# Performance work log

Measured on AMD Instinct MI355X. Metric: run time of the kernel, lower is better.

The kernel has to match this reference:

```python
import jax, jax.numpy as jnp
from jax import lax
import numpy as np


def _box_sum(x, k):
    # zero-padded sliding-window sum over last two dims of [B, H, W];
    # 'SAME' padding with additive identity 0 exactly matches nn.Unfold's
    # zero padding of k//2 on each side for odd k.
    return lax.reduce_window(x, 0.0, lax.add, (1, k, k), (1, 1, 1), 'SAME')


def _local_std(x, k):
    # torch.std over the k*k patch dim is the unbiased (n-1) sample std;
    # fused one-pass form: var = (sum(x^2) - sum(x)^2/n) / (n-1)
    n = float(k * k)
    s1 = _box_sum(x, k)
    s2 = _box_sum(x * x, k)
    var = (s2 - s1 * s1 / n) / (n - 1.0)
    return jnp.sqrt(jnp.maximum(var, 0.0))


def setup_inputs() -> dict:
    key = jax.random.key(0)
    k1, k2 = jax.random.split(key)
    B, C, H, W = 8, 6, 1024, 1024
    predictions = jax.random.normal(k1, (B, C, H, W), dtype=jnp.float32)
    targets = jax.random.randint(k2, (B, H, W), 0, C, dtype=jnp.int64)
    return {"predictions": predictions, "targets": targets, "kernel_size": 5}


def reference(predictions, targets, kernel_size):
    k = int(kernel_size)
    pred_classes = jnp.argmax(predictions, axis=1).astype(jnp.float32)  # [B,H,W]
    tgt = targets.astype(jnp.float32)                                    # [B,H,W]
    pred_consistency = _local_std(pred_classes, k)
    target_consistency = _local_std(tgt, k)
    return jnp.mean((pred_consistency - target_consistency) ** 2)
```

## Files before the change

### kernel.cpp

```cpp
#include <hip/hip_runtime.h>

#define IMG_H 1024
#define IMG_W 1024
#define HW    (IMG_H * IMG_W)
#define HW4   (HW / 4)
#define NCLS  6
#define NBATCH 8
#define TH 8
#define HR 12
#define CSW 1032

__global__ __launch_bounds__(256, 4) void fused_loss_kernel(
    const float* __restrict__ pred, const int* __restrict__ tgt,
    float* __restrict__ out) {
  __shared__ unsigned int halo32[HR * 256];
  __shared__ unsigned int colsum[4 * CSW];
  __shared__ float wsum[4];

  const int tid = threadIdx.x;
  const int job = (blockIdx.x & 7) * 128 + (blockIdx.x >> 3);
  const int img = job >> 7;
  const int y0  = (job & 127) * TH;
  const float* pimg = pred + (size_t)img * NCLS * HW;
  const int*   timg = tgt  + (size_t)img * HW;

  if (tid < 32) {
    const int r = tid >> 3, j = tid & 7;
    colsum[r * CSW + ((j < 4) ? j : 1024 + j)] = 0u;
  }

  for (int k = 0; k < HR * 256; k += 256) {
    const int id  = k + tid;
    const int row = id >> 8;
    const int g   = id & 255;
    const int gy  = y0 + row - 2;
    unsigned int w = 0u;
    if ((unsigned)gy < IMG_H) {
      const float4* p = (const float4*)(pimg + (size_t)gy * IMG_W) + g;
      float4 best = p[0];
      int cx = 0, cy = 0, cz = 0, cw = 0;
#pragma unroll
      for (int c = 1; c < NCLS; ++c) {
        const float4 v = p[(size_t)c * HW4];
        if (v.x > best.x) { best.x = v.x; cx = c; }
        if (v.y > best.y) { best.y = v.y; cy = c; }
        if (v.z > best.z) { best.z = v.z; cz = c; }
        if (v.w > best.w) { best.w = v.w; cw = c; }
      }
      const int4 t4 = *((const int4*)(timg + (size_t)gy * IMG_W) + g);
      w = (unsigned)(cx | (t4.x << 3))
        | ((unsigned)(cy | (t4.y << 3)) << 8)
        | ((unsigned)(cz | (t4.z << 3)) << 16)
        | ((unsigned)(cw | (t4.w << 3)) << 24);
    }
    halo32[row * 256 + g] = w;
  }
  __syncthreads();

  float acc = 0.f;
#pragma unroll
  for (int bb = 0; bb < 2; ++bb) {
    for (int k = 0; k < 4 * 256; k += 256) {
      const int id = k + tid;
      const int r  = id >> 8;
      const int g  = id & 255;
      const unsigned int* h = &halo32[(bb * 4 + r) * 256 + g];
      unsigned s1p[4] = {0,0,0,0}, s2p[4] = {0,0,0,0};
      unsigned s1t[4] = {0,0,0,0}, s2t[4] = {0,0,0,0};
#pragma unroll
      for (int d = 0; d < 5; ++d) {
        const unsigned wv = h[d * 256];
#pragma unroll
        for (int j = 0; j < 4; ++j) {
          const unsigned pv = (wv >> (8 * j)) & 7u;
          const unsigned tv = (wv >> (8 * j + 3)) & 7u;
          s1p[j] += pv; s2p[j] += pv * pv;
          s1t[j] += tv; s2t[j] += tv * tv;
        }
      }
      uint4 o;
      o.x = s1p[0] | (s2p[0] << 8) | (s1t[0] << 16) | (s2t[0] << 24);
      o.y = s1p[1] | (s2p[1] << 8) | (s1t[1] << 16) | (s2t[1] << 24);
      o.z = s1p[2] | (s2p[2] << 8) | (s1t[2] << 16) | (s2t[2] << 24);
      o.w = s1p[3] | (s2p[3] << 8) | (s1t[3] << 16) | (s2t[3] << 24);
      *(uint4*)&colsum[r * CSW + 4 + 4 * g] = o;
    }
    __syncthreads();

    for (int k = 0; k < 4 * 256; k += 256) {
      const int id = k + tid;
      const int r  = id >> 8;
      const int g  = id & 255;
      const unsigned int* cs = &colsum[r * CSW + 4 * g];
      const uint4 wa = *(const uint4*)(cs);
      const uint4 wb = *(const uint4*)(cs + 4);
      const uint4 wc = *(const uint4*)(cs + 8);
      const unsigned w[12] = {wa.x, wa.y, wa.z, wa.w,
                              wb.x, wb.y, wb.z, wb.w,
                              wc.x, wc.y, wc.z, wc.w};
#pragma unroll
      for (int j = 0; j < 4; ++j) {
        int s1p = 0, s2p = 0, s1t = 0, s2t = 0;
#pragma unroll
        for (int d = 0; d < 5; ++d) {
          const unsigned v = w[j + 2 + d];
          s1p += (int)(v & 0xFFu);
          s2p += (int)((v >> 8) & 0xFFu);
          s1t += (int)((v >> 16) & 0xFFu);
          s2t += (int)(v >> 24);
        }
        const float varp = (float)(25 * s2p - s1p * s1p) * (1.0f / 600.0f);
        const float vart = (float)(25 * s2t - s1t * s1t) * (1.0f / 600.0f);
        const float dd = sqrtf(varp) - sqrtf(vart);
        acc += dd * dd;
      }
    }
    __syncthreads();
  }

#pragma unroll
  for (int off = 32; off > 0; off >>= 1) acc += __shfl_down(acc, off, 64);
  const int lane = tid & 63;
  const int wid  = tid >> 6;
  if (lane == 0) wsum[wid] = acc;
  __syncthreads();
  if (tid == 0) {
    const float t = wsum[0] + wsum[1] + wsum[2] + wsum[3];
    atomicAdd(out, t * (1.0f / 8388608.0f));
  }
}

extern "C" void kernel_launch(void* const* d_in, const int* in_sizes, int n_in,
                              void* d_out, int out_size, void* d_ws, size_t ws_size,
                              hipStream_t stream) {
  const float* pred = (const float*)d_in[0];
  const int* tgt    = (const int*)d_in[1];
  float* out = (float*)d_out;
  (void)d_ws; (void)ws_size;

  hipMemsetAsync(d_out, 0, sizeof(float), stream);

  fused_loss_kernel<<<dim3(1024), dim3(256), 0, stream>>>(pred, tgt, out);
}
```

Measured before the change: 330.4 us.

## Split argmax packing into separate streaming kernel before stencil loss

Moves the per-pixel argmax and target packing into a standalone fully parallel kernel that writes one byte per pixel to workspace, then the stencil kernel loads packed words for its halo rows. This removes redundant halo-row argmax and input reads, and lets the bandwidth-heavy pass run as a simple streaming kernel. It adds a second launch and an intermediate buffer write/read.

Measured after the change: 320.0 us. -3.2%, faster.

```diff
diff --git a/kernel.cpp b/kernel.cpp
--- a/kernel.cpp
+++ b/kernel.cpp
@@ -10,19 +10,43 @@
 #define HR 12
 #define CSW 1032
 
-__global__ __launch_bounds__(256, 4) void fused_loss_kernel(
+__global__ __launch_bounds__(256) void argmax_pack_kernel(
     const float* __restrict__ pred, const int* __restrict__ tgt,
-    float* __restrict__ out) {
+    unsigned char* __restrict__ packed) {
+  const int idx = blockIdx.x * 256 + threadIdx.x;
+  const int b   = idx >> 18;
+  const int g   = idx & (HW4 - 1);
+  const float4* p = (const float4*)(pred + (size_t)b * NCLS * HW) + g;
+  float4 best = p[0];
+  int cx = 0, cy = 0, cz = 0, cw = 0;
+#pragma unroll
+  for (int c = 1; c < NCLS; ++c) {
+    const float4 v = p[(size_t)c * HW4];
+    if (v.x > best.x) { best.x = v.x; cx = c; }
+    if (v.y > best.y) { best.y = v.y; cy = c; }
+    if (v.z > best.z) { best.z = v.z; cz = c; }
+    if (v.w > best.w) { best.w = v.w; cw = c; }
+  }
+  const int4 t4 = ((const int4*)(tgt + (size_t)b * HW))[g];
+  uchar4 o;
+  o.x = (unsigned char)(cx | (t4.x << 3));
+  o.y = (unsigned char)(cy | (t4.y << 3));
+  o.z = (unsigned char)(cz | (t4.z << 3));
+  o.w = (unsigned char)(cw | (t4.w << 3));
+  ((uchar4*)packed)[idx] = o;
+}
+
+__global__ __launch_bounds__(256, 4) void stencil_loss_kernel(
+    const unsigned int* __restrict__ packed32, float* __restrict__ out) {
   __shared__ unsigned int halo32[HR * 256];
   __shared__ unsigned int colsum[4 * CSW];
   __shared__ float wsum[4];
 
   const int tid = threadIdx.x;
-  const int job = (blockIdx.x & 7) * 128 + (blockIdx.x >> 3);
+  const int job = blockIdx.x;
   const int img = job >> 7;
   const int y0  = (job & 127) * TH;
-  const float* pimg = pred + (size_t)img * NCLS * HW;
-  const int*   timg = tgt  + (size_t)img * HW;
+  const unsigned int* pw = packed32 + (size_t)img * (HW / 4);
 
   if (tid < 32) {
     const int r = tid >> 3, j = tid & 7;
@@ -35,24 +59,7 @@
     const int g   = id & 255;
     const int gy  = y0 + row - 2;
     unsigned int w = 0u;
-    if ((unsigned)gy < IMG_H) {
-      const float4* p = (const float4*)(pimg + (size_t)gy * IMG_W) + g;
-      float4 best = p[0];
-      int cx = 0, cy = 0, cz = 0, cw = 0;
-#pragma unroll
-      for (int c = 1; c < NCLS; ++c) {
-        const float4 v = p[(size_t)c * HW4];
-        if (v.x > best.x) { best.x = v.x; cx = c; }
-        if (v.y > best.y) { best.y = v.y; cy = c; }
-        if (v.z > best.z) { best.z = v.z; cz = c; }
-        if (v.w > best.w) { best.w = v.w; cw = c; }
-      }
-      const int4 t4 = *((const int4*)(timg + (size_t)gy * IMG_W) + g);
-      w = (unsigned)(cx | (t4.x << 3))
-        | ((unsigned)(cy | (t4.y << 3)) << 8)
-        | ((unsigned)(cz | (t4.z << 3)) << 16)
-        | ((unsigned)(cw | (t4.w << 3)) << 24);
-    }
+    if ((unsigned)gy < IMG_H) w = pw[gy * 256 + g];
     halo32[row * 256 + g] = w;
   }
   __syncthreads();
@@ -136,9 +143,13 @@
   const float* pred = (const float*)d_in[0];
   const int* tgt    = (const int*)d_in[1];
   float* out = (float*)d_out;
-  (void)d_ws; (void)ws_size;
+  unsigned char* packed = (unsigned char*)d_ws;
 
   hipMemsetAsync(d_out, 0, sizeof(float), stream);
 
-  fused_loss_kernel<<<dim3(1024), dim3(256), 0, stream>>>(pred, tgt, out);
+  argmax_pack_kernel<<<dim3(NBATCH * HW4 / 256), dim3(256), 0, stream>>>(
+      pred, tgt, packed);
+
+  stencil_loss_kernel<<<dim3(1024), dim3(256), 0, stream>>>(
+      (const unsigned int*)packed, out);
 }
```
